# Kernel tuning notes

Measured on AMD Instinct MI355X. Metric: run time of the kernel, lower is better.

The kernel has to match this reference:

```python
import jax, jax.numpy as jnp
import numpy as np

N, D, NUM_IDS = 4096, 2048, 256
MARGIN = 0.3


def _pairwise_euclidean(x):
    # torch.cdist(x, x, p=2): safe sqrt of squared distances (zero-grad at 0)
    sq = jnp.sum(x * x, axis=1)                      # [N]
    d2 = sq[:, None] + sq[None, :] - 2.0 * (x @ x.T)  # [N, N]
    d2 = jnp.maximum(d2, 0.0)
    d = jnp.sqrt(jnp.where(d2 > 0.0, d2, 1.0))
    return jnp.where(d2 > 0.0, d, 0.0)


def setup_inputs() -> dict:
    key = jax.random.key(0)
    k1, k2 = jax.random.split(key)
    features = jax.random.normal(k1, (N, D), dtype=jnp.float32)
    labels = jax.random.randint(k2, (N,), 0, NUM_IDS, dtype=jnp.int64)
    return {"features": features, "labels": labels}


def reference(features, labels):
    dist = _pairwise_euclidean(features)                     # [N, N]
    mask_pos = labels[None, :] == labels[:, None]            # [N, N] bool
    # batch-hard mining: hardest positive (max), hardest negative (min)
    dist_ap = jnp.max(jnp.where(mask_pos, dist, 0.0), axis=1)       # [N]
    dist_an = jnp.min(jnp.where(mask_pos, jnp.inf, dist), axis=1)   # [N]
    valid = (dist_ap > 0.0) & jnp.isfinite(dist_an)
    # MarginRankingLoss(dist_an, dist_ap, y=1) = mean(relu(dist_ap - dist_an + margin))
    per_anchor = jnp.maximum(dist_ap - dist_an + MARGIN, 0.0)
    n_valid = jnp.sum(valid)
    loss = jnp.sum(jnp.where(valid, per_anchor, 0.0)) / jnp.maximum(n_valid, 1).astype(per_anchor.dtype)
    return jnp.where(n_valid > 0, loss, 0.0)
```

## Files before the change

kernel.cpp:

```cpp
#include <hip/hip_runtime.h>

#define NN 4096
#define DD 2048
#define MARGIN_F 0.3f
#define NTILES 1056
#define BK 256
#define NIT (DD / BK)
#define QS (127.0f / 6.0f)
#define C2 (2.0f * (6.0f / 127.0f) * (6.0f / 127.0f))

typedef __attribute__((ext_vector_type(4))) int i32x4;

__device__ __forceinline__ unsigned q8(float v) {
    int i = __float2int_rn(v * QS);
    i = min(127, max(-127, i));
    return (unsigned)(i & 255);
}

__global__ __launch_bounds__(256) void prep_kernel(const float* __restrict__ x,
                                                   unsigned char* __restrict__ xq,
                                                   float* __restrict__ sq,
                                                   unsigned int* __restrict__ ap,
                                                   unsigned int* __restrict__ an,
                                                   int* __restrict__ counter) {
    const int wave = threadIdx.x >> 6, lane = threadIdx.x & 63;
    const int row = blockIdx.x * 4 + wave;
    const float* xr = x + (size_t)row * DD;
    unsigned int* orow = (unsigned int*)(xq + (size_t)row * DD);
    float s = 0.0f;
#pragma unroll
    for (int j = 0; j < 8; ++j) {
        float4 v = ((const float4*)xr)[j * 64 + lane];
        s += v.x * v.x + v.y * v.y + v.z * v.z + v.w * v.w;
        orow[j * 64 + lane] = q8(v.x) | (q8(v.y) << 8) | (q8(v.z) << 16) | (q8(v.w) << 24);
    }
    for (int off = 32; off > 0; off >>= 1) s += __shfl_down(s, off, 64);
    if (lane == 0) {
        sq[row] = s;
        ap[row] = 0u;
        an[row] = 0x7F800000u;
    }
    if (threadIdx.x == 0 && blockIdx.x == 0) counter[0] = 0;
}

__global__ __launch_bounds__(256) void gemm_reduce_kernel(
    const unsigned char* __restrict__ xq,
    const float* __restrict__ sq,
    const int* __restrict__ labels,
    unsigned int* __restrict__ ap,
    unsigned int* __restrict__ an,
    int* __restrict__ counter,
    float* __restrict__ out) {
    __shared__ __align__(16) unsigned char As[64 * BK];
    __shared__ __align__(16) unsigned char Bs[128 * BK];

    int rem = blockIdx.x;
    int mi64 = 0;
    while (rem >= 32 - (mi64 >> 1)) { rem -= 32 - (mi64 >> 1); ++mi64; }
    const int nj = (mi64 >> 1) + rem;
    const int row0 = mi64 * 64;
    const int col0 = nj * 128;
    const int phase = blockIdx.x & (NIT - 1);

    const int t = threadIdx.x;
    const int lane = t & 63;
    const int wave = t >> 6;
    const int c = lane & 15;
    const int q = lane >> 4;
    const int wc = wave * 32;

    i32x4 acc[4][2];
#pragma unroll
    for (int mi = 0; mi < 4; ++mi)
#pragma unroll
        for (int ni = 0; ni < 2; ++ni)
            acc[mi][ni] = (i32x4){0, 0, 0, 0};

    const int rowb = t >> 4;
    const int colsw = (t & 15) ^ (rowb & 15);
    const unsigned char* gA[4];
    const unsigned char* gB[8];
#pragma unroll
    for (int s = 0; s < 4; ++s)
        gA[s] = xq + (size_t)(row0 + rowb + 16 * s) * DD + colsw * 16;
#pragma unroll
    for (int s = 0; s < 8; ++s)
        gB[s] = xq + (size_t)(col0 + rowb + 16 * s) * DD + colsw * 16;

    for (int it = 0; it < NIT; ++it) {
        const int k0 = ((it + phase) & (NIT - 1)) * BK;
#pragma unroll
        for (int s = 0; s < 4; ++s)
            __builtin_amdgcn_global_load_lds(
                (const __attribute__((address_space(1))) void*)(gA[s] + k0),
                (__attribute__((address_space(3))) void*)&As[(t + 256 * s) * 16],
                16, 0, 0);
#pragma unroll
        for (int s = 0; s < 8; ++s)
            __builtin_amdgcn_global_load_lds(
                (const __attribute__((address_space(1))) void*)(gB[s] + k0),
                (__attribute__((address_space(3))) void*)&Bs[(t + 256 * s) * 16],
                16, 0, 0);
        __syncthreads();

        const i32x4* Av = (const i32x4*)As;
        const i32x4* Bv = (const i32x4*)Bs;
#pragma unroll
        for (int ks = 0; ks < 4; ++ks) {
            const int kc = q + 4 * ks;
            i32x4 af[4], bfr[2];
#pragma unroll
            for (int mi = 0; mi < 4; ++mi) {
                const int r = mi * 16 + c;
                af[mi] = Av[r * 16 + (kc ^ (r & 15))];
            }
#pragma unroll
            for (int ni = 0; ni < 2; ++ni) {
                const int r = wc + ni * 16 + c;
                bfr[ni] = Bv[r * 16 + (kc ^ (r & 15))];
            }
#pragma unroll
            for (int mi = 0; mi < 4; ++mi)
#pragma unroll
                for (int ni = 0; ni < 2; ++ni)
                    acc[mi][ni] = __builtin_amdgcn_mfma_i32_16x16x64_i8(
                        af[mi], bfr[ni], acc[mi][ni], 0, 0, 0);
        }
        __syncthreads();
    }

    float sq_col[2];
    int lab_col[2];
#pragma unroll
    for (int ni = 0; ni < 2; ++ni) {
        const int gj = col0 + wc + ni * 16 + c;
        sq_col[ni] = sq[gj];
        lab_col[ni] = labels[gj];
    }
    int lab_row[4][4];
    float dist[4][2][4];
#pragma unroll
    for (int mi = 0; mi < 4; ++mi) {
#pragma unroll
        for (int r = 0; r < 4; ++r) {
            const int gi = row0 + mi * 16 + q * 4 + r;
            const float sqi = sq[gi];
            lab_row[mi][r] = labels[gi];
#pragma unroll
            for (int ni = 0; ni < 2; ++ni) {
                float d2 = sqi + sq_col[ni] - C2 * (float)acc[mi][ni][r];
                dist[mi][ni][r] = sqrtf(fmaxf(d2, 0.0f));
            }
        }
    }

#pragma unroll
    for (int mi = 0; mi < 4; ++mi) {
#pragma unroll
        for (int r = 0; r < 4; ++r) {
            const int gi = row0 + mi * 16 + q * 4 + r;
            const int li = lab_row[mi][r];
            float apm = 0.0f;
            float anm = __builtin_inff();
#pragma unroll
            for (int ni = 0; ni < 2; ++ni) {
                const int gj = col0 + wc + ni * 16 + c;
                const float d = dist[mi][ni][r];
                if (li == lab_col[ni]) {
                    if (gi != gj) apm = fmaxf(apm, d);
                } else {
                    anm = fminf(anm, d);
                }
            }
#pragma unroll
            for (int off = 1; off < 16; off <<= 1) {
                apm = fmaxf(apm, __shfl_xor(apm, off, 16));
                anm = fminf(anm, __shfl_xor(anm, off, 16));
            }
            if (c == 0) {
                atomicMax(&ap[gi], __float_as_uint(apm));
                atomicMin(&an[gi], __float_as_uint(anm));
            }
        }
    }

#pragma unroll
    for (int ni = 0; ni < 2; ++ni) {
        const int gj = col0 + wc + ni * 16 + c;
        const int lj = lab_col[ni];
        float apm = 0.0f;
        float anm = __builtin_inff();
#pragma unroll
        for (int mi = 0; mi < 4; ++mi) {
#pragma unroll
            for (int r = 0; r < 4; ++r) {
                const int gi = row0 + mi * 16 + q * 4 + r;
                const float d = dist[mi][ni][r];
                if (lj == lab_row[mi][r]) {
                    if (gi != gj) apm = fmaxf(apm, d);
                } else {
                    anm = fminf(anm, d);
                }
            }
        }
        apm = fmaxf(apm, __shfl_xor(apm, 16, 64));
        anm = fminf(anm, __shfl_xor(anm, 16, 64));
        apm = fmaxf(apm, __shfl_xor(apm, 32, 64));
        anm = fminf(anm, __shfl_xor(anm, 32, 64));
        if (q == 0) {
            atomicMax(&ap[gj], __float_as_uint(apm));
            atomicMin(&an[gj], __float_as_uint(anm));
        }
    }

    __syncthreads();
    int* flag = (int*)As;
    if (t == 0) {
        int old = __hip_atomic_fetch_add(counter, 1, __ATOMIC_ACQ_REL,
                                         __HIP_MEMORY_SCOPE_AGENT);
        flag[0] = (old == NTILES - 1) ? 1 : 0;
    }
    __syncthreads();
    if (flag[0]) {
        float sum = 0.0f;
        int cnt = 0;
        for (int i = t; i < NN; i += 256) {
            const float a = __uint_as_float(__hip_atomic_load(
                &ap[i], __ATOMIC_RELAXED, __HIP_MEMORY_SCOPE_AGENT));
            const float b = __uint_as_float(__hip_atomic_load(
                &an[i], __ATOMIC_RELAXED, __HIP_MEMORY_SCOPE_AGENT));
            if ((a > 0.0f) && (b < __builtin_inff())) {
                sum += fmaxf(a - b + MARGIN_F, 0.0f);
                cnt += 1;
            }
        }
        for (int off = 32; off > 0; off >>= 1) {
            sum += __shfl_down(sum, off, 64);
            cnt += __shfl_down(cnt, off, 64);
        }
        float* ssum = (float*)Bs;
        int* scnt = (int*)Bs + 8;
        if (lane == 0) { ssum[wave] = sum; scnt[wave] = cnt; }
        __syncthreads();
        if (t == 0) {
            float s = 0.0f; int n = 0;
#pragma unroll
            for (int w = 0; w < 4; ++w) { s += ssum[w]; n += scnt[w]; }
            out[0] = (n > 0) ? s / (float)n : 0.0f;
        }
    }
}

extern "C" void kernel_launch(void* const* d_in, const int* in_sizes, int n_in,
                              void* d_out, int out_size, void* d_ws, size_t ws_size,
                              hipStream_t stream) {
    const float* x = (const float*)d_in[0];
    const int* labels = (const int*)d_in[1];
    float* out = (float*)d_out;

    char* ws = (char*)d_ws;
    unsigned char* xq = (unsigned char*)ws;
    float* sq = (float*)(ws + (size_t)NN * DD);
    unsigned int* ap = (unsigned int*)(ws + (size_t)NN * DD + (size_t)NN * 4);
    unsigned int* an = (unsigned int*)(ws + (size_t)NN * DD + (size_t)NN * 8);
    int* counter = (int*)(ws + (size_t)NN * DD + (size_t)NN * 12);

    prep_kernel<<<NN / 4, 256, 0, stream>>>(x, xq, sq, ap, an, counter);
    gemm_reduce_kernel<<<NTILES, 256, 0, stream>>>(xq, sq, labels, ap, an, counter, out);
}
```

Measured before the change: 141.8 us.

## Double-buffer int8 LDS tiles with BK=128 to overlap loads and MFMA

```diff
diff --git a/kernel.cpp b/kernel.cpp
--- a/kernel.cpp
+++ b/kernel.cpp
@@ -4,7 +4,7 @@
 #define DD 2048
 #define MARGIN_F 0.3f
 #define NTILES 1056
-#define BK 256
+#define BK 128
 #define NIT (DD / BK)
 #define QS (127.0f / 6.0f)
 #define C2 (2.0f * (6.0f / 127.0f) * (6.0f / 127.0f))
@@ -51,8 +51,8 @@
     unsigned int* __restrict__ an,
     int* __restrict__ counter,
     float* __restrict__ out) {
-    __shared__ __align__(16) unsigned char As[64 * BK];
-    __shared__ __align__(16) unsigned char Bs[128 * BK];
+    __shared__ __align__(16) unsigned char As[2][64 * BK];
+    __shared__ __align__(16) unsigned char Bs[2][128 * BK];
 
     int rem = blockIdx.x;
     int mi64 = 0;
@@ -76,56 +76,66 @@
         for (int ni = 0; ni < 2; ++ni)
             acc[mi][ni] = (i32x4){0, 0, 0, 0};
 
-    const int rowb = t >> 4;
-    const int colsw = (t & 15) ^ (rowb & 15);
-    const unsigned char* gA[4];
-    const unsigned char* gB[8];
+    const int rowb = t >> 3;
+    const int colsw = (t & 7) ^ (rowb & 7);
+    const unsigned char* gA[2];
+    const unsigned char* gB[4];
+#pragma unroll
+    for (int s = 0; s < 2; ++s)
+        gA[s] = xq + (size_t)(row0 + rowb + 32 * s) * DD + colsw * 16;
 #pragma unroll
     for (int s = 0; s < 4; ++s)
-        gA[s] = xq + (size_t)(row0 + rowb + 16 * s) * DD + colsw * 16;
-#pragma unroll
-    for (int s = 0; s < 8; ++s)
-        gB[s] = xq + (size_t)(col0 + rowb + 16 * s) * DD + colsw * 16;
-
-    for (int it = 0; it < NIT; ++it) {
+        gB[s] = xq + (size_t)(col0 + rowb + 32 * s) * DD + colsw * 16;
+
+    auto stage = [&](int buf, int it) {
         const int k0 = ((it + phase) & (NIT - 1)) * BK;
+#pragma unroll
+        for (int s = 0; s < 2; ++s)
+            __builtin_amdgcn_global_load_lds(
+                (const __attribute__((address_space(1))) void*)(gA[s] + k0),
+                (__attribute__((address_space(3))) void*)&As[buf][(t + 256 * s) * 16],
+                16, 0, 0);
 #pragma unroll
         for (int s = 0; s < 4; ++s)
             __builtin_amdgcn_global_load_lds(
-                (const __attribute__((address_space(1))) void*)(gA[s] + k0),
-                (__attribute__((address_space(3))) void*)&As[(t + 256 * s) * 16],
+                (const __attribute__((address_space(1))) void*)(gB[s] + k0),
+                (__attribute__((address_space(3))) void*)&Bs[buf][(t + 256 * s) * 16],
                 16, 0, 0);
-#pragma unroll
-        for (int s = 0; s < 8; ++s)
-            __builtin_amdgcn_global_load_lds(
-                (const __attribute__((address_space(1))) void*)(gB[s] + k0),
-                (__attribute__((address_space(3))) void*)&Bs[(t + 256 * s) * 16],
-                16, 0, 0);
-        __syncthreads();
-
-        const i32x4* Av = (const i32x4*)As;
-        const i32x4* Bv = (const i32x4*)Bs;
-#pragma unroll
-        for (int ks = 0; ks < 4; ++ks) {
-            const int kc = q + 4 * ks;
-            i32x4 af[4], bfr[2];
+    };
+
+    stage(0, 0);
+    __syncthreads();
+    for (int it = 0; it < NIT; ++it) {
+        const int cur = it & 1;
+        const i32x4* Av = (const i32x4*)As[cur];
+        const i32x4* Bv = (const i32x4*)Bs[cur];
+
+        i32x4 af[2][4], bfr[2][2];
+#pragma unroll
+        for (int h = 0; h < 2; ++h) {
 #pragma unroll
             for (int mi = 0; mi < 4; ++mi) {
                 const int r = mi * 16 + c;
-                af[mi] = Av[r * 16 + (kc ^ (r & 15))];
+                af[h][mi] = Av[r * 8 + ((q + 4 * h) ^ (r & 7))];
             }
 #pragma unroll
             for (int ni = 0; ni < 2; ++ni) {
                 const int r = wc + ni * 16 + c;
-                bfr[ni] = Bv[r * 16 + (kc ^ (r & 15))];
-            }
+                bfr[h][ni] = Bv[r * 8 + ((q + 4 * h) ^ (r & 7))];
+            }
+        }
+
+        if (it + 1 < NIT) stage(cur ^ 1, it + 1);
+
+#pragma unroll
+        for (int h = 0; h < 2; ++h)
 #pragma unroll
             for (int mi = 0; mi < 4; ++mi)
 #pragma unroll
                 for (int ni = 0; ni < 2; ++ni)
                     acc[mi][ni] = __builtin_amdgcn_mfma_i32_16x16x64_i8(
-                        af[mi], bfr[ni], acc[mi][ni], 0, 0, 0);
-        }
+                        af[h][mi], bfr[h][ni], acc[mi][ni], 0, 0, 0);
+
         __syncthreads();
     }
 
```

Result: no change. 144.5 us (+1.9%).
